# Kernel optimization log

Measured on AMD Instinct MI355X. Metric: run time of the kernel, lower is better.

The kernel has to match this reference:

```python
import jax, jax.numpy as jnp
import numpy as np

H = 16
DH = 64
THETA = 10000.0


def setup_inputs() -> dict:
    key = jax.random.key(0)
    ks = jax.random.split(key, 9)
    B, M, R = 4, 1024, 256
    d = H * DH
    s = 0.05
    return {
        "Pq": jax.random.normal(ks[0], (B, M, R), jnp.float32) * s,
        "Pk": jax.random.normal(ks[1], (B, M, R), jnp.float32) * s,
        "Pv": jax.random.normal(ks[2], (B, M, R), jnp.float32) * s,
        "Vq": jax.random.normal(ks[3], (R, d), jnp.float32) * s,
        "Vk": jax.random.normal(ks[4], (R, d), jnp.float32) * s,
        "Vv": jax.random.normal(ks[5], (R, d), jnp.float32) * s,
        "bq": jax.random.normal(ks[6], (d,), jnp.float32) * s,
        "bk": jax.random.normal(ks[7], (d,), jnp.float32) * s,
        "bv": jax.random.normal(ks[8], (d,), jnp.float32) * s,
        "attention_mask": jnp.ones((B, M), jnp.int32),
        "position_ids": jnp.tile(jnp.arange(M, dtype=jnp.int32), (B, 1)),
    }


def _rope_cos_sin(position_ids):
    # half-dim frequencies, matching the kernel's half-half rotation
    half = DH // 2
    inv_freq = 1.0 / (THETA ** (jnp.arange(0, half, dtype=jnp.float32) / half))
    ang = position_ids.astype(jnp.float32)[..., None] * inv_freq  # [B,M,half]
    return jnp.cos(ang), jnp.sin(ang)


def _rotate(x, cos, sin):
    # x: [B,H,M,dh]; cos/sin: [B,M,half] -> broadcast over heads
    half = DH // 2
    x0, x1 = x[..., :half], x[..., half:]
    c = cos[:, None, :, :]
    s = sin[:, None, :, :]
    return jnp.concatenate([x0 * c - x1 * s, x0 * s + x1 * c], axis=-1)


def reference(Pq, Pk, Pv, Vq, Vk, Vv, bq, bk, bv, attention_mask, position_ids):
    B, M, R = Pq.shape
    # reconstruct per-head Q/K/V from low-rank factors
    Vq3 = Vq.reshape(R, H, DH)
    Vk3 = Vk.reshape(R, H, DH)
    Vv3 = Vv.reshape(R, H, DH)
    q = jnp.einsum("bmr,rhd->bhmd", Pq, Vq3) + bq.reshape(H, DH)[None, :, None, :]
    k = jnp.einsum("bmr,rhd->bhmd", Pk, Vk3) + bk.reshape(H, DH)[None, :, None, :]
    v = jnp.einsum("bmr,rhd->bhmd", Pv, Vv3) + bv.reshape(H, DH)[None, :, None, :]
    cos, sin = _rope_cos_sin(position_ids)
    q = _rotate(q, cos, sin)
    k = _rotate(k, cos, sin)
    scale = 1.0 / jnp.sqrt(jnp.float32(DH))
    scores = jnp.einsum("bhmd,bhnd->bhmn", q, k) * scale  # [B,H,M,M]
    valid = attention_mask.astype(bool)
    pad = valid[:, None, :, None] & valid[:, None, None, :]
    scores = jnp.where(pad, scores, -jnp.inf)
    p = jax.nn.softmax(scores, axis=-1)
    out = jnp.einsum("bhmn,bhnd->bhmd", p, v)
    return out
```

## Files before the change

kernel.cpp:

```cpp
#include <hip/hip_runtime.h>
#include <hip/hip_bf16.h>
#include <math.h>

#define BB 4
#define MM 1024
#define RR 256
#define HH 16
#define DHH 64
#define DD (HH*DHH)

typedef __attribute__((ext_vector_type(8))) short short8;
typedef __attribute__((ext_vector_type(4))) float f32x4;

#if defined(__has_builtin)
#  if __has_builtin(__builtin_amdgcn_exp2f)
#    define EXP2F(x) __builtin_amdgcn_exp2f(x)
#  endif
#endif
#ifndef EXP2F
#  define EXP2F(x) __expf((x) * 0.6931471805599453f)
#endif

static __device__ __forceinline__ unsigned pack_bf16_rh(float a, float b) {
    unsigned ua = __builtin_bit_cast(unsigned, a) + 0x8000u;
    unsigned ub = __builtin_bit_cast(unsigned, b) + 0x8000u;
    return __builtin_amdgcn_perm(ub, ua, 0x07060302u);
}
static __device__ __forceinline__ unsigned short bf_rh(float a) {
    return (unsigned short)((__builtin_bit_cast(unsigned, a) + 0x8000u) >> 16);
}

__global__ __launch_bounds__(256) void prep_kernel(
    const float* __restrict__ Vq, const float* __restrict__ Vk, const float* __restrict__ Vv,
    __hip_bfloat16* __restrict__ VTq, __hip_bfloat16* __restrict__ VTk,
    __hip_bfloat16* __restrict__ VTv)
{
    const int t   = threadIdx.x;
    const int z   = blockIdx.x / 256;
    const int rem = blockIdx.x % 256;
    const int r0  = (rem & 7) * 32;
    const int d0  = (rem >> 3) * 32;
    const float* V = (z == 0) ? Vq : (z == 1) ? Vk : Vv;
    __hip_bfloat16* VT = (z == 0) ? VTq : (z == 1) ? VTk : VTv;

    __shared__ __hip_bfloat16 Ts[32][33];
    {
        const int row = t >> 3;
        const int c4  = (t & 7) * 4;
        float4 f = *(const float4*)&V[(size_t)(r0 + row) * DD + d0 + c4];
        Ts[row][c4 + 0] = __float2bfloat16(f.x);
        Ts[row][c4 + 1] = __float2bfloat16(f.y);
        Ts[row][c4 + 2] = __float2bfloat16(f.z);
        Ts[row][c4 + 3] = __float2bfloat16(f.w);
    }
    __syncthreads();
    {
        const int orow = t >> 3;
        const int oc4  = (t & 7) * 4;
        union { unsigned short u[4]; uint2 v; } pk;
        #pragma unroll
        for (int i = 0; i < 4; ++i) pk.u[i] = *(unsigned short*)&Ts[oc4 + i][orow];
        *(uint2*)&VT[(size_t)(d0 + orow) * RR + r0 + oc4] = pk.v;
    }
}

__global__ __launch_bounds__(256, 4) void svd_gemm(
    const float* __restrict__ Pq, const float* __restrict__ Pk, const float* __restrict__ Pv,
    const __hip_bfloat16* __restrict__ VTq, const __hip_bfloat16* __restrict__ VTk,
    const __hip_bfloat16* __restrict__ VTv,
    const float* __restrict__ bq, const float* __restrict__ bk, const float* __restrict__ bv,
    const int* __restrict__ pos_ids,
    __hip_bfloat16* __restrict__ qout, __hip_bfloat16* __restrict__ kout,
    __hip_bfloat16* __restrict__ vTout)
{
    const int which = blockIdx.z;
    const float* P           = (which == 0) ? Pq : (which == 1) ? Pk : Pv;
    const __hip_bfloat16* VT = (which == 0) ? VTq : (which == 1) ? VTk : VTv;
    const float* bias        = (which == 0) ? bq : (which == 1) ? bk : bv;

    const int hg  = blockIdx.y;
    const int bm0 = blockIdx.x * 64;
    const int b   = bm0 >> 10;
    const int m0  = bm0 & 1023;
    const int tid = threadIdx.x;
    const int lane = tid & 63;
    const int w    = tid >> 6;
    const int l15  = lane & 15;
    const int quad = lane >> 4;

    __shared__ alignas(16) short Bs[128 * 72];

    f32x4 acc[8];
    #pragma unroll
    for (int dt = 0; dt < 8; ++dt) acc[dt] = (f32x4){0.f, 0.f, 0.f, 0.f};

    const float* prow = P + (size_t)(bm0 + w * 16 + l15) * RR;

    #pragma unroll
    for (int kc = 0; kc < 4; ++kc) {
        #pragma unroll
        for (int i = 0; i < 4; ++i) {
            int u   = tid + i * 256;
            int row = u >> 3;
            int cg  = (u & 7) * 8;
            *(uint4*)&Bs[row * 72 + cg] =
                *(const uint4*)((const short*)VT + (size_t)(hg * 128 + row) * RR + kc * 64 + cg);
        }
        __syncthreads();

        #pragma unroll
        for (int ks = 0; ks < 2; ++ks) {
            const int ko = kc * 64 + ks * 32 + quad * 8;
            float4 alo = *(const float4*)(prow + ko);
            float4 ahi = *(const float4*)(prow + ko + 4);
            union { unsigned u[4]; short8 s; } pa;
            pa.u[0] = pack_bf16_rh(alo.x, alo.y);
            pa.u[1] = pack_bf16_rh(alo.z, alo.w);
            pa.u[2] = pack_bf16_rh(ahi.x, ahi.y);
            pa.u[3] = pack_bf16_rh(ahi.z, ahi.w);
            #pragma unroll
            for (int dt = 0; dt < 8; ++dt) {
                short8 bf = *(const short8*)&Bs[(dt * 16 + l15) * 72 + ks * 32 + quad * 8];
                acc[dt] = __builtin_amdgcn_mfma_f32_16x16x32_bf16(pa.s, bf, acc[dt], 0, 0, 0);
            }
        }
        __syncthreads();
    }

    #pragma unroll
    for (int dt = 0; dt < 8; ++dt) {
        float bc = bias[hg * 128 + dt * 16 + l15];
        #pragma unroll
        for (int r = 0; r < 4; ++r) acc[dt][r] += bc;
    }

    if (which < 2) {
        __hip_bfloat16* out = (which == 0) ? qout : kout;
        int pm[4];
        #pragma unroll
        for (int r = 0; r < 4; ++r) pm[r] = pos_ids[bm0 + w * 16 + quad * 4 + r];
        float cB[2][4], sB[2][4];
        #pragma unroll
        for (int f2 = 0; f2 < 2; ++f2) {
            float invf = __powf(10000.0f, -(float)(f2 * 16 + l15) * (1.0f / 32.0f));
            #pragma unroll
            for (int r = 0; r < 4; ++r)
                __sincosf((float)pm[r] * invf, &sB[f2][r], &cB[f2][r]);
        }
        short* Ls = Bs;
        #pragma unroll
        for (int dt = 0; dt < 8; ++dt) {
            const int f2 = dt & 1;
            #pragma unroll
            for (int r = 0; r < 4; ++r) {
                float x  = acc[dt][r], xp = acc[dt ^ 2][r];
                float c = cB[f2][r], s = sB[f2][r];
                float val = ((dt & 3) < 2) ? (x * c - xp * s) : (xp * s + x * c);
                Ls[(w * 16 + quad * 4 + r) * 136 + dt * 16 + l15] = (short)bf_rh(val);
            }
        }
        __syncthreads();
        #pragma unroll
        for (int i = 0; i < 4; ++i) {
            int u   = tid + i * 256;
            int ml  = u >> 4;
            int hh  = (u >> 3) & 1;
            int seg = u & 7;
            *(uint4*)&out[(((size_t)b * HH + hg * 2 + hh) * MM + m0 + ml) * DHH + seg * 8] =
                *(const uint4*)&Ls[ml * 136 + hh * 64 + seg * 8];
        }
    } else {
        short* Tt = Bs;
        #pragma unroll
        for (int dt = 0; dt < 8; ++dt) {
            uint2 pk;
            pk.x = pack_bf16_rh(acc[dt][0], acc[dt][1]);
            pk.y = pack_bf16_rh(acc[dt][2], acc[dt][3]);
            *(uint2*)&Tt[(dt * 16 + l15) * 72 + w * 16 + quad * 4] = pk;
        }
        __syncthreads();
        #pragma unroll
        for (int i = 0; i < 4; ++i) {
            int u   = tid + i * 256;
            int row = u >> 3;
            int seg = u & 7;
            int h   = hg * 2 + (row >> 6);
            int din = row & 63;
            *(uint4*)&vTout[(((size_t)b * HH + h) * DHH + din) * MM + m0 + seg * 8] =
                *(const uint4*)&Tt[row * 72 + seg * 8];
        }
    }
}

__global__ __launch_bounds__(256, 4) void attn_kernel(
    const __hip_bfloat16* __restrict__ q, const __hip_bfloat16* __restrict__ k,
    const __hip_bfloat16* __restrict__ vT,
    const int* __restrict__ mask, float* __restrict__ out)
{
    const int bh    = blockIdx.x & 63;
    const int qt    = blockIdx.x >> 6;
    const int b     = bh >> 4;
    const int tid   = threadIdx.x;
    const int lane  = tid & 63;
    const int w     = tid >> 6;
    const int mhalf = w & 1;
    const int khalf = w >> 1;
    const int l15   = lane & 15;
    const int quad  = lane >> 4;
    const int q0    = qt * 64;
    const int koff  = khalf * 64;

    __shared__ alignas(16) __hip_bfloat16 Kt[128][72];
    __shared__ alignas(16) __hip_bfloat16 Vt[64][136];

    const short* kbase = (const short*)k  + (size_t)bh * MM * DHH;
    const short* vbase = (const short*)vT + (size_t)bh * DHH * MM;

    short8 qa[2][2];
    #pragma unroll
    for (int mt = 0; mt < 2; ++mt) {
        const short* qb = (const short*)q +
            ((size_t)bh * MM + q0 + mhalf * 32 + mt * 16 + l15) * DHH + quad * 8;
        qa[mt][0] = *(const short8*)(qb);
        qa[mt][1] = *(const short8*)(qb + 32);
    }

    f32x4 Ot[2][4];
    #pragma unroll
    for (int mt = 0; mt < 2; ++mt)
        #pragma unroll
        for (int dt = 0; dt < 4; ++dt) Ot[mt][dt] = (f32x4){0.f, 0.f, 0.f, 0.f};
    float lsum[2] = {0.f, 0.f};

    const int* maskb = mask + b * MM;
    const int srcbase = (lane & 48) | ((lane & 48) >> 2);
    const float k2 = 0.125f * 1.44269504089f;

    for (int nc = 0; nc < MM / 128; ++nc) {
        const int n0 = nc * 128;
        #pragma unroll
        for (int pass = 0; pass < 4; ++pass) {
            int u   = tid + pass * 256;
            int row = u >> 3;
            int cg  = u & 7;
            *(uint4*)&Kt[row][cg * 8] =
                *(const uint4*)(kbase + (size_t)(n0 + row) * DHH + cg * 8);
        }
        #pragma unroll
        for (int pass = 0; pass < 4; ++pass) {
            int u   = tid + pass * 256;
            int row = u >> 4;
            int c   = u & 15;
            union { uint4 q4; uint2 h2[2]; } vld;
            vld.q4 = *(const uint4*)(vbase + (size_t)row * MM + n0 + c * 8);
            int g  = c >> 3;
            int c6 = c & 7;
            int base0 = g * 64 + (c6 >> 2) * 32 + (c6 & 1) * 16 + ((c6 >> 1) & 1) * 4;
            *(uint2*)&Vt[row][base0]     = vld.h2[0];
            *(uint2*)&Vt[row][base0 + 8] = vld.h2[1];
        }
        __syncthreads();

        unsigned long long bal = __ballot(maskb[n0 + koff + lane] != 0);

        f32x4 S[2][4];
        #pragma unroll
        for (int t = 0; t < 4; ++t) {
            const short* kr = (const short*)&Kt[koff + t * 16 + l15][quad * 8];
            short8 ka0 = *(const short8*)(kr);
            short8 ka1 = *(const short8*)(kr + 32);
            #pragma unroll
            for (int mt = 0; mt < 2; ++mt) {
                f32x4 c = (f32x4){0.f, 0.f, 0.f, 0.f};
                c = __builtin_amdgcn_mfma_f32_16x16x32_bf16(ka0, qa[mt][0], c, 0, 0, 0);
                c = __builtin_amdgcn_mfma_f32_16x16x32_bf16(ka1, qa[mt][1], c, 0, 0, 0);
                S[mt][t] = c;
            }
        }

        #pragma unroll
        for (int t = 0; t < 4; ++t) {
            unsigned bits = (unsigned)(bal >> (t * 16 + quad * 4));
            #pragma unroll
            for (int r = 0; r < 4; ++r) {
                float sb = ((bits >> r) & 1u) ? 0.0f : -1e30f;
                #pragma unroll
                for (int mt = 0; mt < 2; ++mt) {
                    float e = EXP2F(fmaf(S[mt][t][r], k2, sb));
                    lsum[mt] += e;
                    S[mt][t][r] = e;
                }
            }
        }

        short8 pa[2][2];
        #pragma unroll
        for (int mt = 0; mt < 2; ++mt)
            #pragma unroll
            for (int p = 0; p < 2; ++p) {
                union { unsigned u[4]; short8 s; } pk;
                pk.u[0] = pack_bf16_rh(S[mt][2*p][0],   S[mt][2*p][1]);
                pk.u[1] = pack_bf16_rh(S[mt][2*p][2],   S[mt][2*p][3]);
                pk.u[2] = pack_bf16_rh(S[mt][2*p+1][0], S[mt][2*p+1][1]);
                pk.u[3] = pack_bf16_rh(S[mt][2*p+1][2], S[mt][2*p+1][3]);
                pa[mt][p] = pk.s;
            }

        #pragma unroll
        for (int p = 0; p < 2; ++p) {
            #pragma unroll
            for (int dt = 0; dt < 4; ++dt) {
                short8 vb = *(const short8*)&Vt[dt * 16 + l15][koff + p * 32 + quad * 8];
                #pragma unroll
                for (int mt = 0; mt < 2; ++mt)
                    Ot[mt][dt] = __builtin_amdgcn_mfma_f32_16x16x32_bf16(pa[mt][p], vb, Ot[mt][dt], 0, 0, 0);
            }
        }
        __syncthreads();
    }

    float* C = (float*)&Kt[0][0];
    const int cb = (mhalf * 64 + lane) * 34;
    if (khalf == 1) {
        #pragma unroll
        for (int mt = 0; mt < 2; ++mt) {
            #pragma unroll
            for (int dt = 0; dt < 4; ++dt)
                #pragma unroll
                for (int r = 0; r < 4; ++r)
                    C[cb + mt * 16 + dt * 4 + r] = Ot[mt][dt][r];
            C[cb + 32 + mt] = lsum[mt];
        }
    }
    __syncthreads();
    if (khalf == 0) {
        #pragma unroll
        for (int mt = 0; mt < 2; ++mt) {
            #pragma unroll
            for (int dt = 0; dt < 4; ++dt)
                #pragma unroll
                for (int r = 0; r < 4; ++r)
                    Ot[mt][dt][r] += C[cb + mt * 16 + dt * 4 + r];
            lsum[mt] += C[cb + 32 + mt];
        }
        #pragma unroll
        for (int mt = 0; mt < 2; ++mt) {
            float s = lsum[mt];
            s += __shfl_xor(s, 16, 64);
            s += __shfl_xor(s, 32, 64);
            float inv = 1.0f / s;
            float* ob = out + ((size_t)bh * MM + q0 + mhalf * 32 + mt * 16) * DHH;
            #pragma unroll
            for (int r = 0; r < 4; ++r) {
                float ir = __shfl(inv, srcbase + r, 64);
                #pragma unroll
                for (int dt = 0; dt < 4; ++dt)
                    ob[(quad * 4 + r) * DHH + dt * 16 + l15] = Ot[mt][dt][r] * ir;
            }
        }
    }
}

extern "C" void kernel_launch(void* const* d_in, const int* in_sizes, int n_in,
                              void* d_out, int out_size, void* d_ws, size_t ws_size,
                              hipStream_t stream) {
    const float* Pq = (const float*)d_in[0];
    const float* Pk = (const float*)d_in[1];
    const float* Pv = (const float*)d_in[2];
    const float* Vq = (const float*)d_in[3];
    const float* Vk = (const float*)d_in[4];
    const float* Vv = (const float*)d_in[5];
    const float* bq = (const float*)d_in[6];
    const float* bk = (const float*)d_in[7];
    const float* bv = (const float*)d_in[8];
    const int* mask = (const int*)d_in[9];
    const int* pos  = (const int*)d_in[10];
    float* out = (float*)d_out;

    const size_t qkv_elems = (size_t)BB * HH * MM * DHH;
    __hip_bfloat16* qb  = (__hip_bfloat16*)d_ws;
    __hip_bfloat16* kb  = qb + qkv_elems;
    __hip_bfloat16* vT  = kb + qkv_elems;
    __hip_bfloat16* VTq = vT + qkv_elems;
    __hip_bfloat16* VTk = VTq + (size_t)DD * RR;
    __hip_bfloat16* VTv = VTk + (size_t)DD * RR;

    prep_kernel<<<768, 256, 0, stream>>>(Vq, Vk, Vv, VTq, VTk, VTv);

    dim3 gG(BB * MM / 64, HH / 2, 3);
    svd_gemm<<<gG, 256, 0, stream>>>(Pq, Pk, Pv, VTq, VTk, VTv, bq, bk, bv, pos,
                                     qb, kb, vT);

    attn_kernel<<<BB * HH * (MM / 64), 256, 0, stream>>>(qb, kb, vT, mask, out);
}
```

Before: 139.1 us.

## Enlarge svd_gemm M-tile to 128 rows and read B fragments directly from global

```diff
diff --git a/kernel.cpp b/kernel.cpp
--- a/kernel.cpp
+++ b/kernel.cpp
@@ -64,7 +64,7 @@
     }
 }
 
-__global__ __launch_bounds__(256, 4) void svd_gemm(
+__global__ __launch_bounds__(256) void svd_gemm(
     const float* __restrict__ Pq, const float* __restrict__ Pk, const float* __restrict__ Pv,
     const __hip_bfloat16* __restrict__ VTq, const __hip_bfloat16* __restrict__ VTk,
     const __hip_bfloat16* __restrict__ VTv,
@@ -79,7 +79,7 @@
     const float* bias        = (which == 0) ? bq : (which == 1) ? bk : bv;
 
     const int hg  = blockIdx.y;
-    const int bm0 = blockIdx.x * 64;
+    const int bm0 = blockIdx.x * 128;
     const int b   = bm0 >> 10;
     const int m0  = bm0 & 1023;
     const int tid = threadIdx.x;
@@ -88,80 +88,87 @@
     const int l15  = lane & 15;
     const int quad = lane >> 4;
 
-    __shared__ alignas(16) short Bs[128 * 72];
-
-    f32x4 acc[8];
+    __shared__ alignas(16) short EP[128 * 136];
+
+    f32x4 acc[2][8];
     #pragma unroll
-    for (int dt = 0; dt < 8; ++dt) acc[dt] = (f32x4){0.f, 0.f, 0.f, 0.f};
-
-    const float* prow = P + (size_t)(bm0 + w * 16 + l15) * RR;
+    for (int mt = 0; mt < 2; ++mt)
+        #pragma unroll
+        for (int dt = 0; dt < 8; ++dt) acc[mt][dt] = (f32x4){0.f, 0.f, 0.f, 0.f};
+
+    const float* prow0 = P + (size_t)(bm0 + w * 32 + l15) * RR;
+    const float* prow1 = prow0 + 16 * RR;
+    const short* vtbase = (const short*)VT + (size_t)hg * 128 * RR;
 
     #pragma unroll
-    for (int kc = 0; kc < 4; ++kc) {
-        #pragma unroll
-        for (int i = 0; i < 4; ++i) {
-            int u   = tid + i * 256;
-            int row = u >> 3;
-            int cg  = (u & 7) * 8;
-            *(uint4*)&Bs[row * 72 + cg] =
-                *(const uint4*)((const short*)VT + (size_t)(hg * 128 + row) * RR + kc * 64 + cg);
-        }
-        __syncthreads();
-
-        #pragma unroll
-        for (int ks = 0; ks < 2; ++ks) {
-            const int ko = kc * 64 + ks * 32 + quad * 8;
-            float4 alo = *(const float4*)(prow + ko);
-            float4 ahi = *(const float4*)(prow + ko + 4);
-            union { unsigned u[4]; short8 s; } pa;
-            pa.u[0] = pack_bf16_rh(alo.x, alo.y);
-            pa.u[1] = pack_bf16_rh(alo.z, alo.w);
-            pa.u[2] = pack_bf16_rh(ahi.x, ahi.y);
-            pa.u[3] = pack_bf16_rh(ahi.z, ahi.w);
-            #pragma unroll
-            for (int dt = 0; dt < 8; ++dt) {
-                short8 bf = *(const short8*)&Bs[(dt * 16 + l15) * 72 + ks * 32 + quad * 8];
-                acc[dt] = __builtin_amdgcn_mfma_f32_16x16x32_bf16(pa.s, bf, acc[dt], 0, 0, 0);
-            }
-        }
-        __syncthreads();
+    for (int ks = 0; ks < 8; ++ks) {
+        const int ko = ks * 32 + quad * 8;
+        float4 a0lo = *(const float4*)(prow0 + ko);
+        float4 a0hi = *(const float4*)(prow0 + ko + 4);
+        float4 a1lo = *(const float4*)(prow1 + ko);
+        float4 a1hi = *(const float4*)(prow1 + ko + 4);
+        union { unsigned u[4]; short8 s; } pa0, pa1;
+        pa0.u[0] = pack_bf16_rh(a0lo.x, a0lo.y);
+        pa0.u[1] = pack_bf16_rh(a0lo.z, a0lo.w);
+        pa0.u[2] = pack_bf16_rh(a0hi.x, a0hi.y);
+        pa0.u[3] = pack_bf16_rh(a0hi.z, a0hi.w);
+        pa1.u[0] = pack_bf16_rh(a1lo.x, a1lo.y);
+        pa1.u[1] = pack_bf16_rh(a1lo.z, a1lo.w);
+        pa1.u[2] = pack_bf16_rh(a1hi.x, a1hi.y);
+        pa1.u[3] = pack_bf16_rh(a1hi.z, a1hi.w);
+
+        #pragma unroll
+        for (int dt = 0; dt < 8; ++dt) {
+            short8 bf = *(const short8*)(vtbase + (size_t)(dt * 16 + l15) * RR + ko);
+            acc[0][dt] = __builtin_amdgcn_mfma_f32_16x16x32_bf16(pa0.s, bf, acc[0][dt], 0, 0, 0);
+            acc[1][dt] = __builtin_amdgcn_mfma_f32_16x16x32_bf16(pa1.s, bf, acc[1][dt], 0, 0, 0);
+        }
     }
 
     #pragma unroll
     for (int dt = 0; dt < 8; ++dt) {
         float bc = bias[hg * 128 + dt * 16 + l15];
         #pragma unroll
-        for (int r = 0; r < 4; ++r) acc[dt][r] += bc;
+        for (int mt = 0; mt < 2; ++mt)
+            #pragma unroll
+            for (int r = 0; r < 4; ++r) acc[mt][dt][r] += bc;
     }
 
     if (which < 2) {
         __hip_bfloat16* out = (which == 0) ? qout : kout;
-        int pm[4];
-        #pragma unroll
-        for (int r = 0; r < 4; ++r) pm[r] = pos_ids[bm0 + w * 16 + quad * 4 + r];
-        float cB[2][4], sB[2][4];
+        int pm[2][4];
+        #pragma unroll
+        for (int r = 0; r < 4; ++r) {
+            pm[0][r] = pos_ids[bm0 + w * 32 + quad * 4 + r];
+            pm[1][r] = pos_ids[bm0 + w * 32 + 16 + quad * 4 + r];
+        }
+        float cB[2][2][4], sB[2][2][4];
         #pragma unroll
         for (int f2 = 0; f2 < 2; ++f2) {
             float invf = __powf(10000.0f, -(float)(f2 * 16 + l15) * (1.0f / 32.0f));
             #pragma unroll
-            for (int r = 0; r < 4; ++r)
-                __sincosf((float)pm[r] * invf, &sB[f2][r], &cB[f2][r]);
-        }
-        short* Ls = Bs;
-        #pragma unroll
-        for (int dt = 0; dt < 8; ++dt) {
-            const int f2 = dt & 1;
-            #pragma unroll
-            for (int r = 0; r < 4; ++r) {
-                float x  = acc[dt][r], xp = acc[dt ^ 2][r];
-                float c = cB[f2][r], s = sB[f2][r];
-                float val = ((dt & 3) < 2) ? (x * c - xp * s) : (xp * s + x * c);
-                Ls[(w * 16 + quad * 4 + r) * 136 + dt * 16 + l15] = (short)bf_rh(val);
-            }
-        }
+            for (int mt = 0; mt < 2; ++mt)
+                #pragma unroll
+                for (int r = 0; r < 4; ++r)
+                    __sincosf((float)pm[mt][r] * invf, &sB[f2][mt][r], &cB[f2][mt][r]);
+        }
+        short* Ls = EP;
+        #pragma unroll
+        for (int mt = 0; mt < 2; ++mt)
+            #pragma unroll
+            for (int dt = 0; dt < 8; ++dt) {
+                const int f2 = dt & 1;
+                #pragma unroll
+                for (int r = 0; r < 4; ++r) {
+                    float x  = acc[mt][dt][r], xp = acc[mt][dt ^ 2][r];
+                    float c = cB[f2][mt][r], s = sB[f2][mt][r];
+                    float val = ((dt & 3) < 2) ? (x * c - xp * s) : (xp * s + x * c);
+                    Ls[(w * 32 + mt * 16 + quad * 4 + r) * 136 + dt * 16 + l15] = (short)bf_rh(val);
+                }
+            }
         __syncthreads();
         #pragma unroll
-        for (int i = 0; i < 4; ++i) {
+        for (int i = 0; i < 8; ++i) {
             int u   = tid + i * 256;
             int ml  = u >> 4;
             int hh  = (u >> 3) & 1;
@@ -170,24 +177,26 @@
                 *(const uint4*)&Ls[ml * 136 + hh * 64 + seg * 8];
         }
     } else {
-        short* Tt = Bs;
-        #pragma unroll
-        for (int dt = 0; dt < 8; ++dt) {
-            uint2 pk;
-            pk.x = pack_bf16_rh(acc[dt][0], acc[dt][1]);
-            pk.y = pack_bf16_rh(acc[dt][2], acc[dt][3]);
-            *(uint2*)&Tt[(dt * 16 + l15) * 72 + w * 16 + quad * 4] = pk;
-        }
+        short* Tt = EP;
+        #pragma unroll
+        for (int dt = 0; dt < 8; ++dt)
+            #pragma unroll
+            for (int mt = 0; mt < 2; ++mt) {
+                uint2 pk;
+                pk.x = pack_bf16_rh(acc[mt][dt][0], acc[mt][dt][1]);
+                pk.y = pack_bf16_rh(acc[mt][dt][2], acc[mt][dt][3]);
+                *(uint2*)&Tt[(dt * 16 + l15) * 136 + w * 32 + mt * 16 + quad * 4] = pk;
+            }
         __syncthreads();
         #pragma unroll
-        for (int i = 0; i < 4; ++i) {
+        for (int i = 0; i < 8; ++i) {
             int u   = tid + i * 256;
-            int row = u >> 3;
-            int seg = u & 7;
+            int row = u >> 4;
+            int seg = u & 15;
             int h   = hg * 2 + (row >> 6);
             int din = row & 63;
             *(uint4*)&vTout[(((size_t)b * HH + h) * DHH + din) * MM + m0 + seg * 8] =
-                *(const uint4*)&Tt[row * 72 + seg * 8];
+                *(const uint4*)&Tt[row * 136 + seg * 8];
         }
     }
 }
@@ -387,7 +396,7 @@
 
     prep_kernel<<<768, 256, 0, stream>>>(Vq, Vk, Vv, VTq, VTk, VTv);
 
-    dim3 gG(BB * MM / 64, HH / 2, 3);
+    dim3 gG(BB * MM / 128, HH / 2, 3);
     svd_gemm<<<gG, 256, 0, stream>>>(Pq, Pk, Pv, VTq, VTk, VTv, bq, bk, bv, pos,
                                      qb, kb, vT);
 
```

After: 152.5 us. 9.6% more time.
